# Kernel optimization log

Measured on AMD Instinct MI355X. Metric: run time of the kernel, lower is better.

The kernel has to match this reference:

```python
import jax, jax.numpy as jnp
import numpy as np

K = 20          # knn
EPS = 1e-5      # InstanceNorm2d eps
NEG_SLOPE = 0.2 # LeakyReLU slope


def setup_inputs() -> dict:
    key = jax.random.key(0)
    k1, k2 = jax.random.split(key)
    B, C, N = 4, 64, 4096
    out_dim, in_dim = 64, 2 * C
    batch = jax.random.normal(k1, (B, C, N), dtype=jnp.float32)
    # Conv2d(in_dim, out_dim, kernel_size=1, bias=False) weight, squeezed to [out,in]
    W = jax.random.normal(k2, (out_dim, in_dim), dtype=jnp.float32) * (1.0 / np.sqrt(in_dim))
    return {"batch": batch, "W": W}


def reference(batch, W):
    x = batch  # [B, C, N]
    # --- KNNGraph: pairwise squared distances + top-k nearest ---
    xx = jnp.sum(x * x, axis=1)                      # [B, N]
    inner = jnp.einsum('bcn,bcm->bnm', x, x)         # [B, N, N]
    neg_dist = -(xx[:, :, None] - 2.0 * inner + xx[:, None, :])  # [B, N, N]
    _, idx = jax.lax.top_k(neg_dist, K)              # [B, N, K] nearest neighbors
    # --- edge feature gather: concat(x_j - x_i, x_i) -> [B, 2C, N, K] ---
    nbr = jax.vmap(lambda xb, ib: xb[:, ib])(x, idx) # [B, C, N, K]
    center = x[:, :, :, None]                        # [B, C, N, 1]
    edge = jnp.concatenate([nbr - center, jnp.broadcast_to(center, nbr.shape)], axis=1)
    # --- 1x1 Conv2d (shared MLP, no bias) ---
    y = jnp.einsum('oc,bcnk->bonk', W, edge)         # [B, out, N, K]
    # --- InstanceNorm2d (no affine, biased var over spatial dims) ---
    mean = jnp.mean(y, axis=(2, 3), keepdims=True)
    var = jnp.var(y, axis=(2, 3), keepdims=True)
    y = (y - mean) * jax.lax.rsqrt(var + EPS)
    # --- LeakyReLU(0.2) ---
    y = jnp.where(y >= 0, y, NEG_SLOPE * y)
    # --- MaxPool over neighbor dim ---
    return jnp.max(y, axis=3)                        # [B, out, N]
```

## Files before the change

### kernel.cpp

```cpp
#include <hip/hip_runtime.h>
#include <hip/hip_bf16.h>
#include <cstdint>
#include <cstddef>

#define BB 4
#define NN 4096
#define NROW (BB*NN)
#define CAP3 512
#define ZSTAR 2.17f
#define SLACK 0.40

typedef float v2f   __attribute__((ext_vector_type(2)));
typedef float f32x16 __attribute__((ext_vector_type(16)));
typedef short s16x8 __attribute__((ext_vector_type(8)));
typedef _Float16 f16x8 __attribute__((ext_vector_type(8)));

__device__ __forceinline__ v2f pkfma(v2f a, v2f b, v2f c) {
  return __builtin_elementwise_fma(a, b, c);
}

__device__ __forceinline__ unsigned long long sort64(unsigned long long S, int lane) {
  #pragma unroll
  for (int kk = 2; kk <= 64; kk <<= 1) {
    #pragma unroll
    for (int j = kk >> 1; j > 0; j >>= 1) {
      unsigned long long o = __shfl_xor(S, j);
      bool up    = ((lane & kk) == 0);
      bool lower = ((lane & j) == 0);
      unsigned long long mn = (S < o) ? S : o;
      unsigned long long mx = (S < o) ? o : S;
      S = (lower == up) ? mn : mx;
    }
  }
  return S;
}
__device__ __forceinline__ unsigned long long merge_low64(
    unsigned long long L, unsigned long long S, int lane) {
  unsigned long long Sr = __shfl(S, 63 - lane);
  unsigned long long lo = (L < Sr) ? L : Sr;
  #pragma unroll
  for (int j = 32; j > 0; j >>= 1) {
    unsigned long long o = __shfl_xor(lo, j);
    unsigned long long mn = (lo < o) ? lo : o;
    unsigned long long mx = (lo < o) ? o : lo;
    lo = ((lane & j) == 0) ? mn : mx;
  }
  return lo;
}

__global__ __launch_bounds__(256) void k1_prep(
    const float* __restrict__ x, const float* __restrict__ W,
    float* __restrict__ xT, unsigned short* __restrict__ xh2,
    double* __restrict__ xxd, float* __restrict__ Trow,
    float* __restrict__ uT, float* __restrict__ vT)
{
  __shared__ float xc[64][65];
  __shared__ float xr[64][68];
  __shared__ float w1[64][65];
  __shared__ float wd[64][65];
  int t = threadIdx.x;
  int b  = blockIdx.x >> 6;
  int n0 = (blockIdx.x & 63) * 64;

  for (int i = t; i < 4096; i += 256) {
    int o = i >> 6, c = i & 63;
    float a = W[o*128 + c];
    w1[o][c] = a;
    wd[o][c] = W[o*128 + 64 + c] - a;
  }
  for (int i = t; i < 4096; i += 256) {
    int c = i >> 6, n = i & 63;
    xc[c][n] = x[((size_t)b*64 + c)*4096 + n0 + n];
  }
  __syncthreads();

  for (int i = t; i < 4096; i += 256) {
    int n = i >> 6, c = i & 63;
    float v = xc[c][n];
    xr[n][c] = v;
    size_t pt = (size_t)b*4096 + n0 + n;
    xT[pt*64 + c] = v;
    xh2[pt*80 + c] = __builtin_bit_cast(unsigned short, (_Float16)v);
  }
  if (t < 64) {
    int n = t;
    float s0=0,s1=0,s2=0,s3=0; double sd=0.0;
    for (int c = 0; c < 64; c += 4) {
      float a0=xc[c][n],a1=xc[c+1][n],a2=xc[c+2][n],a3=xc[c+3][n];
      s0=fmaf(a0,a0,s0); s1=fmaf(a1,a1,s1); s2=fmaf(a2,a2,s2); s3=fmaf(a3,a3,s3);
      sd += (double)a0*a0 + (double)a1*a1 + (double)a2*a2 + (double)a3*a3;
    }
    float xxv = (s0+s1)+(s2+s3);
    size_t ri = (size_t)b*4096 + n0 + n;
    xxd[ri] = sd;
    Trow[ri] = fmaf(-ZSTAR, sqrtf(fmaf(4.0f, xxv, 128.0f)), 64.0f);
    size_t xb2 = ri*80 + 64;
    xh2[xb2] = __builtin_bit_cast(unsigned short, (_Float16)xxv);
    #pragma unroll
    for (int q = 1; q < 16; ++q) xh2[xb2 + q] = 0;
  }
  v2f w1r[32], wdr[32];
  int o = t & 63;
  #pragma unroll
  for (int j = 0; j < 32; ++j) {
    w1r[j].x = w1[o][2*j]; w1r[j].y = w1[o][2*j+1];
    wdr[j].x = wd[o][2*j]; wdr[j].y = wd[o][2*j+1];
  }
  __syncthreads();

  for (int i = t; i < 4096; i += 256) {
    int n = i >> 6;
    v2f au; au.x=0.f; au.y=0.f;
    v2f av; av.x=0.f; av.y=0.f;
    #pragma unroll
    for (int cb = 0; cb < 16; ++cb) {
      float4 xv = *(const float4*)&xr[n][cb*4];
      v2f p0; p0.x = xv.x; p0.y = xv.y;
      v2f p1; p1.x = xv.z; p1.y = xv.w;
      au = pkfma(w1r[2*cb],   p0, au);
      au = pkfma(w1r[2*cb+1], p1, au);
      av = pkfma(wdr[2*cb],   p0, av);
      av = pkfma(wdr[2*cb+1], p1, av);
    }
    size_t idx = ((size_t)b*4096 + n0 + n)*64 + o;
    uT[idx] = au.x + au.y;
    vT[idx] = av.x + av.y;
  }
}

__global__ __launch_bounds__(256) void k2_screen(
    const unsigned short* __restrict__ xh2, const float* __restrict__ Trow,
    unsigned* __restrict__ bitmap)
{
  int t  = threadIdx.x;
  int nblk = blockIdx.x >> 3;
  int ms   = blockIdx.x & 7;
  int row0 = nblk * 128;
  int b = row0 >> 12;
  int wv = t >> 6, lane = t & 63;
  int lr = lane & 31, oct = lane >> 5;
  int n = row0 + wv*32 + lr;

  s16x8 bn[5];
  #pragma unroll
  for (int ks = 0; ks < 4; ++ks)
    bn[ks] = *(const s16x8*)(xh2 + (size_t)n*80 + ks*16 + oct*8);
  {
    s16x8 z;
    #pragma unroll
    for (int q = 0; q < 8; ++q) z[q] = 0;
    if (!oct) z[0] = (short)0xB800;
    bn[4] = z;
  }
  float cn = -0.5f * Trow[n];

  const unsigned short* xmB = xh2 + (size_t)b*4096*80;
  int mbase = ms * 512;

  for (int mt = 0; mt < 8; ++mt) {
    int m0 = mbase + mt*64;
    s16x8 am0[5], am1[5];
    #pragma unroll
    for (int ks = 0; ks < 4; ++ks) {
      am0[ks] = *(const s16x8*)(xmB + (size_t)(m0 + lr)*80      + ks*16 + oct*8);
      am1[ks] = *(const s16x8*)(xmB + (size_t)(m0 + 32 + lr)*80 + ks*16 + oct*8);
    }
    am0[4] = *(const s16x8*)(xmB + (size_t)(m0 + lr)*80      + 64 + oct*8);
    am1[4] = *(const s16x8*)(xmB + (size_t)(m0 + 32 + lr)*80 + 64 + oct*8);

    f32x16 a0, a1;
    #pragma unroll
    for (int i = 0; i < 16; ++i) { a0[i] = 0.f; a1[i] = 0.f; }
    #pragma unroll
    for (int ks = 0; ks < 5; ++ks) {
      f16x8 B = __builtin_bit_cast(f16x8, bn[ks]);
      a0 = __builtin_amdgcn_mfma_f32_32x32x16_f16(
             __builtin_bit_cast(f16x8, am0[ks]), B, a0, 0, 0, 0);
      a1 = __builtin_amdgcn_mfma_f32_32x32x16_f16(
             __builtin_bit_cast(f16x8, am1[ks]), B, a1, 0, 0, 0);
    }

    unsigned ua[4] = {0u,0u,0u,0u}, ub[4] = {0u,0u,0u,0u};
    #pragma unroll
    for (int i = 0; i < 16; ++i) {
      int p = (i & 3) + 8*(i >> 2) + 4*oct;
      unsigned bit = 1u << p;
      ua[i & 3] = (a0[i] > cn) ? (ua[i & 3] | bit) : ua[i & 3];
      ub[i & 3] = (a1[i] > cn) ? (ub[i & 3] | bit) : ub[i & 3];
    }
    unsigned u0 = (ua[0] | ua[1]) | (ua[2] | ua[3]);
    unsigned u1 = (ub[0] | ub[1]) | (ub[2] | ub[3]);
    unsigned w0 = u0 | (unsigned)__shfl_xor((int)u0, 32);
    unsigned w1 = u1 | (unsigned)__shfl_xor((int)u1, 32);
    bitmap[(size_t)n*128 + ms*16 + mt*2 + oct] = oct ? w1 : w0;
  }
}

__global__ __launch_bounds__(256) void k3_select(
    const float* __restrict__ xT, const double* __restrict__ xxd,
    const float* __restrict__ Trow, const unsigned* __restrict__ bitmap,
    const float* __restrict__ uT, const float* __restrict__ vT,
    float* __restrict__ stage, double* __restrict__ pS1, double* __restrict__ pS2,
    unsigned* __restrict__ slowcnt, unsigned* __restrict__ slowlist)
{
  __shared__ unsigned short candm[4][CAP3];
  int wv = threadIdx.x >> 6, lane = threadIdx.x & 63;
  int row = blockIdx.x * 4 + wv;
  int b = row >> 12;

  double s1t = 0.0, s2t = 0.0;
  double xxn = xxd[row];

  uint2 wds = *(const uint2*)&bitmap[(size_t)row*128 + lane*2];
  int myc = __popc(wds.x) + __popc(wds.y);
  int inc = myc;
  #pragma unroll
  for (int d = 1; d < 64; d <<= 1) {
    int v = __shfl_up(inc, d);
    if (lane >= d) inc += v;
  }
  int total = __shfl(inc, 63);
  int off = inc - myc;
  bool slow = (total < 20) || (total > CAP3);

  if (!slow) {
    unsigned w = wds.x; int mb = lane*64;
    while (w) { int j = __ffs(w) - 1; w &= w - 1;
                candm[wv][off++] = (unsigned short)(mb + j); }
    w = wds.y; mb = lane*64 + 32;
    while (w) { int j = __ffs(w) - 1; w &= w - 1;
                candm[wv][off++] = (unsigned short)(mb + j); }
  }
  __builtin_amdgcn_wave_barrier();

  if (!slow) {
    const float* pn = xT + (size_t)row*64;
    int nr = (total + 63) >> 6;
    unsigned long long L = ~0ull;
    for (int r = 0; r < nr; ++r) {
      int ci = r*64 + lane;
      unsigned long long S = ~0ull;
      if (ci < total) {
        int m = (int)candm[wv][ci];
        const float* pm = xT + ((size_t)b*4096 + m)*64;
        double acc0 = 0.0, acc1 = 0.0;
        #pragma unroll
        for (int c5 = 0; c5 < 64; c5 += 4) {
          float4 A = *(const float4*)(pn + c5);
          float4 B = *(const float4*)(pm + c5);
          acc0 = fma((double)A.x, (double)B.x, acc0);
          acc1 = fma((double)A.y, (double)B.y, acc1);
          acc0 = fma((double)A.z, (double)B.z, acc0);
          acc1 = fma((double)A.w, (double)B.w, acc1);
        }
        double d = xxn + xxd[(size_t)b*4096 + m] - 2.0*(acc0 + acc1);
        d = fmax(d, 0.0);
        S = (((unsigned long long)__double_as_longlong(d)) & ~0xFFFull)
          | (unsigned long long)m;
      }
      S = sort64(S, lane);
      L = (r == 0) ? S : merge_low64(L, S, lane);
    }
    unsigned long long k19 = __shfl(L, 19);
    double d20 = __longlong_as_double((long long)(k19 & ~0xFFFull));
    float Tr = Trow[row];
    if (!(d20 - xxn < (double)Tr - SLACK)) {
      slow = true;
    } else {
      int mlow = (int)(L & 0xFFFull);
      const float* ub = uT + (size_t)b*4096*64;
      float mx = -3.4e38f, s1 = 0.f, s2 = 0.f;
      #pragma unroll
      for (int k = 0; k < 20; ++k) {
        int m = __shfl(mlow, k);
        float g = ub[(size_t)m*64 + lane];
        mx = fmaxf(mx, g); s1 += g; s2 = fmaf(g, g, s2);
      }
      size_t ro = (size_t)row*64 + lane;
      float v = vT[ro];
      stage[ro] = mx + v;
      double dv = (double)v;
      s1t = (double)s1 + 20.0*dv;
      s2t = (double)s2 + 2.0*dv*(double)s1 + 20.0*dv*dv;
    }
  }
  if (slow && lane == 0) {
    unsigned i = atomicAdd(slowcnt, 1u); slowlist[i] = row;
  }
  pS1[(size_t)row*64 + lane] = s1t;
  pS2[(size_t)row*64 + lane] = s2t;
}

__global__ __launch_bounds__(256) void k3b_slow(
    const float* __restrict__ xT, const double* __restrict__ xxd,
    const unsigned* __restrict__ slowcnt, const unsigned* __restrict__ slowlist,
    const float* __restrict__ uT, const float* __restrict__ vT,
    float* __restrict__ stage, double* __restrict__ k3bS1, double* __restrict__ k3bS2)
{
  __shared__ unsigned long long wtop[4][64];
  __shared__ unsigned long long pend[4][64];
  __shared__ unsigned t20[20];
  unsigned nslow = *slowcnt;
  int t = threadIdx.x, wv = t >> 6, lane = t & 63;
  for (unsigned ii = blockIdx.x; ii < nslow; ii += gridDim.x) {
    int row = (int)slowlist[ii];
    int b = row >> 12, n = row & 4095;
    const float* pn = xT + ((size_t)b*4096 + n)*64;
    double xxn = xxd[(size_t)b*4096 + n];

    unsigned long long L;
    unsigned long long kth;
    int pc = 0;
    for (int r = 0; r < 16; ++r) {
      int m = wv*1024 + r*64 + lane;
      const float* pm = xT + ((size_t)b*4096 + m)*64;
      double acc0 = 0.0, acc1 = 0.0;
      #pragma unroll
      for (int c5 = 0; c5 < 64; c5 += 4) {
        float4 A = *(const float4*)(pn + c5);
        float4 B = *(const float4*)(pm + c5);
        acc0 = fma((double)A.x, (double)B.x, acc0);
        acc1 = fma((double)A.y, (double)B.y, acc1);
        acc0 = fma((double)A.z, (double)B.z, acc0);
        acc1 = fma((double)A.w, (double)B.w, acc1);
      }
      double d = xxn + xxd[(size_t)b*4096 + m] - 2.0*(acc0 + acc1);
      d = fmax(d, 0.0);
      unsigned long long S =
          (((unsigned long long)__double_as_longlong(d)) & ~0xFFFull)
        | (unsigned long long)m;
      if (r == 0) {
        L = sort64(S, lane);
        kth = __shfl(L, 63);
        continue;
      }
      bool take = (S < kth);
      unsigned long long mk = __ballot(take);
      int cnt = __popcll(mk);
      if (pc + cnt > 64) {
        __builtin_amdgcn_wave_barrier();
        unsigned long long P = (lane < pc) ? pend[wv][lane] : ~0ull;
        P = sort64(P, lane);
        L = merge_low64(L, P, lane);
        kth = __shfl(L, 63);
        pc = 0;
      }
      if (take) {
        int pos = pc + __popcll(mk & ((1ull << lane) - 1ull));
        pend[wv][pos] = S;
      }
      pc += cnt;
      __builtin_amdgcn_wave_barrier();
    }
    if (pc > 0) {
      __builtin_amdgcn_wave_barrier();
      unsigned long long P = (lane < pc) ? pend[wv][lane] : ~0ull;
      P = sort64(P, lane);
      L = merge_low64(L, P, lane);
    }
    wtop[wv][lane] = L;
    __syncthreads();
    if (wv == 0) {
      unsigned long long m01 = merge_low64(wtop[0][lane],
                                           wtop[1][lane], lane);
      unsigned long long m23 = merge_low64(wtop[2][lane],
                                           wtop[3][lane], lane);
      unsigned long long F = merge_low64(m01, m23, lane);
      if (lane < 20) t20[lane] = (unsigned)(F & 0xFFFull);
    }
    __syncthreads();
    if (t < 64) {
      const float* ub = uT + (size_t)b*4096*64;
      float mx = -3.4e38f, s1 = 0.f, s2 = 0.f;
      #pragma unroll
      for (int k = 0; k < 20; ++k) {
        unsigned m = t20[k];
        float g = ub[(size_t)m*64 + t];
        mx = fmaxf(mx, g); s1 += g; s2 = fmaf(g, g, s2);
      }
      size_t ro = ((size_t)b*4096 + n)*64 + t;
      float v = vT[ro];
      stage[ro] = mx + v;
      double dv = (double)v;
      __hip_atomic_fetch_add(&k3bS1[b*64 + t], (double)s1 + 20.0*dv,
                             __ATOMIC_RELAXED, __HIP_MEMORY_SCOPE_AGENT);
      __hip_atomic_fetch_add(&k3bS2[b*64 + t], (double)s2 + 2.0*dv*(double)s1 + 20.0*dv*dv,
                             __ATOMIC_RELAXED, __HIP_MEMORY_SCOPE_AGENT);
    }
    __syncthreads();
  }
}

__global__ __launch_bounds__(256) void k4a1_reduce(
    const double* __restrict__ pS1, const double* __restrict__ pS2,
    double* __restrict__ part1, double* __restrict__ part2)
{
  __shared__ double r1[4][64], r2[4][64];
  int blk = blockIdx.x;
  int t = threadIdx.x, wv = t >> 6, o = t & 63;
  size_t rbase = (size_t)blk*64 + wv*16;
  double s1 = 0.0, s2 = 0.0;
  for (int j = 0; j < 16; ++j) {
    s1 += pS1[(rbase + j)*64 + o];
    s2 += pS2[(rbase + j)*64 + o];
  }
  r1[wv][o] = s1; r2[wv][o] = s2;
  __syncthreads();
  if (wv == 0) {
    part1[(size_t)blk*64 + o] = r1[0][o]+r1[1][o]+r1[2][o]+r1[3][o];
    part2[(size_t)blk*64 + o] = r2[0][o]+r2[1][o]+r2[2][o]+r2[3][o];
  }
}

__global__ __launch_bounds__(256) void k4a2_params(
    const double* __restrict__ part1, const double* __restrict__ part2,
    const double* __restrict__ k3bS1, const double* __restrict__ k3bS2,
    float2* __restrict__ params)
{
  __shared__ double r1[4][64], r2[4][64];
  int b = blockIdx.x;
  int t = threadIdx.x, wv = t >> 6, o = t & 63;
  double s1 = 0.0, s2 = 0.0;
  for (int j = wv*16; j < wv*16 + 16; ++j) {
    s1 += part1[((size_t)b*64 + j)*64 + o];
    s2 += part2[((size_t)b*64 + j)*64 + o];
  }
  r1[wv][o] = s1; r2[wv][o] = s2;
  __syncthreads();
  if (wv == 0) {
    double S1 = k3bS1[b*64 + o] + r1[0][o]+r1[1][o]+r1[2][o]+r1[3][o];
    double S2 = k3bS2[b*64 + o] + r2[0][o]+r2[1][o]+r2[2][o]+r2[3][o];
    double inv = 1.0 / (4096.0 * 20.0);
    double mean = S1 * inv;
    double var  = S2 * inv - mean * mean;
    float2 pr; pr.x = (float)mean; pr.y = (float)rsqrt(var + 1e-5);
    params[b*64 + o] = pr;
  }
}

__global__ __launch_bounds__(256) void k4b_final(
    const float* __restrict__ stage, const float2* __restrict__ params,
    float* __restrict__ out)
{
  __shared__ float tile[64][65];
  int blk = blockIdx.x;
  int b = blk >> 6, n0 = (blk & 63) * 64;
  int t = threadIdx.x;
  int o = t & 63;
  float2 pr = params[b*64 + o];
  for (int i = t; i < 4096; i += 256) {
    int nn = i >> 6;
    float y = (stage[((size_t)b*4096 + n0 + nn)*64 + o] - pr.x) * pr.y;
    tile[nn][o] = (y >= 0.f) ? y : 0.2f * y;
  }
  __syncthreads();
  for (int i = t; i < 4096; i += 256) {
    int oo = i >> 6, nn = i & 63;
    out[((size_t)(b*64 + oo))*4096 + n0 + nn] = tile[nn][oo];
  }
}

extern "C" void kernel_launch(void* const* d_in, const int* in_sizes, int n_in,
                              void* d_out, int out_size, void* d_ws, size_t ws_size,
                              hipStream_t stream)
{
  (void)in_sizes; (void)n_in; (void)out_size; (void)ws_size;
  const float* x = (const float*)d_in[0];
  const float* W = (const float*)d_in[1];
  float* out = (float*)d_out;

  char* ws = (char*)d_ws;
  size_t off = 0;
  auto alloc = [&](size_t bytes) {
    char* p = ws + off;
    off = (off + bytes + 255) & ~(size_t)255;
    return p;
  };
  float*          uT       = (float*)         alloc((size_t)NROW*64*4);
  float*          vT       = (float*)         alloc((size_t)NROW*64*4);
  float*          xT       = (float*)         alloc((size_t)NROW*64*4);
  float*          stage    = (float*)         alloc((size_t)NROW*64*4);
  unsigned short* xh2      = (unsigned short*)alloc((size_t)NROW*80*2);
  double*         xxd      = (double*)        alloc((size_t)NROW*8);
  float*          Trow     = (float*)         alloc((size_t)NROW*4);
  double*         pS1      = (double*)        alloc((size_t)NROW*64*8);
  double*         pS2      = (double*)        alloc((size_t)NROW*64*8);
  double*         part1    = (double*)        alloc((size_t)256*64*8);
  double*         part2    = (double*)        alloc((size_t)256*64*8);
  unsigned*       bitmap   = (unsigned*)      alloc((size_t)NROW*128*4);
  float2*         params   = (float2*)        alloc(256*8);
  unsigned*       slowcnt  = (unsigned*)      alloc(256);
  double*         k3bS1    = (double*)        alloc(256*8);
  double*         k3bS2    = (double*)        alloc(256*8);
  unsigned*       slowlist = (unsigned*)      alloc((size_t)NROW*4);

  hipMemsetAsync(slowcnt, 0, 256 + 2048 + 2048, stream);

  k1_prep    <<<256,  256, 0, stream>>>(x, W, xT, xh2, xxd, Trow, uT, vT);
  k2_screen  <<<1024, 256, 0, stream>>>(xh2, Trow, bitmap);
  k3_select  <<<4096, 256, 0, stream>>>(xT, xxd, Trow, bitmap, uT, vT,
                                        stage, pS1, pS2, slowcnt, slowlist);
  k3b_slow   <<<512,  256, 0, stream>>>(xT, xxd, slowcnt, slowlist,
                                        uT, vT, stage, k3bS1, k3bS2);
  k4a1_reduce<<<256,  256, 0, stream>>>(pS1, pS2, part1, part2);
  k4a2_params<<<4,    256, 0, stream>>>(part1, part2, k3bS1, k3bS2, params);
  k4b_final  <<<256,  256, 0, stream>>>(stage, params, out);
}
```

Baseline: 150.3 us.

## Fold slow-path full scan into select kernel, drop separate slow kernel

The separate k3b_slow kernel, its slow-row list, atomics and memset are removed. Rows that fail the candidate screen now fall back inside k3_select to a per-wave full 4096-point scan using a threshold-filtered pending buffer. This saves one kernel launch, a memset and the atomic accumulation of statistics. The cost is that a slow row is now scanned by a single wave rather than a whole block, which can lengthen the tail if many rows fail. The candidate path also switches from sort-and-merge on every round to threshold filtering.

```diff
diff --git a/kernel.cpp b/kernel.cpp
--- a/kernel.cpp
+++ b/kernel.cpp
@@ -200,16 +200,16 @@
     const float* __restrict__ xT, const double* __restrict__ xxd,
     const float* __restrict__ Trow, const unsigned* __restrict__ bitmap,
     const float* __restrict__ uT, const float* __restrict__ vT,
-    float* __restrict__ stage, double* __restrict__ pS1, double* __restrict__ pS2,
-    unsigned* __restrict__ slowcnt, unsigned* __restrict__ slowlist)
+    float* __restrict__ stage, double* __restrict__ pS1, double* __restrict__ pS2)
 {
   __shared__ unsigned short candm[4][CAP3];
+  __shared__ unsigned long long pend[4][64];
   int wv = threadIdx.x >> 6, lane = threadIdx.x & 63;
   int row = blockIdx.x * 4 + wv;
   int b = row >> 12;
 
-  double s1t = 0.0, s2t = 0.0;
   double xxn = xxd[row];
+  const double* xxb = xxd + (size_t)b*4096;
 
   uint2 wds = *(const uint2*)&bitmap[(size_t)row*128 + lane*2];
   int myc = __popc(wds.x) + __popc(wds.y);
@@ -221,9 +221,9 @@
   }
   int total = __shfl(inc, 63);
   int off = inc - myc;
-  bool slow = (total < 20) || (total > CAP3);
-
-  if (!slow) {
+  bool fullscan = (total < 20) || (total > CAP3);
+
+  if (!fullscan) {
     unsigned w = wds.x; int mb = lane*64;
     while (w) { int j = __ffs(w) - 1; w &= w - 1;
                 candm[wv][off++] = (unsigned short)(mb + j); }
@@ -233,15 +233,20 @@
   }
   __builtin_amdgcn_wave_barrier();
 
-  if (!slow) {
-    const float* pn = xT + (size_t)row*64;
-    int nr = (total + 63) >> 6;
-    unsigned long long L = ~0ull;
+  const float* pn = xT + (size_t)row*64;
+  unsigned long long L = ~0ull;
+
+  for (int attempt = 0; attempt < 2; ++attempt) {
+    int ncand = fullscan ? 4096 : total;
+    int nr = (ncand + 63) >> 6;
+    unsigned long long kth = ~0ull;
+    int pc = 0;
+    L = ~0ull;
     for (int r = 0; r < nr; ++r) {
       int ci = r*64 + lane;
       unsigned long long S = ~0ull;
-      if (ci < total) {
-        int m = (int)candm[wv][ci];
+      if (ci < ncand) {
+        int m = fullscan ? ci : (int)candm[wv][ci];
         const float* pm = xT + ((size_t)b*4096 + m)*64;
         double acc0 = 0.0, acc1 = 0.0;
         #pragma unroll
@@ -253,82 +258,11 @@
           acc0 = fma((double)A.z, (double)B.z, acc0);
           acc1 = fma((double)A.w, (double)B.w, acc1);
         }
-        double d = xxn + xxd[(size_t)b*4096 + m] - 2.0*(acc0 + acc1);
+        double d = xxn + xxb[m] - 2.0*(acc0 + acc1);
         d = fmax(d, 0.0);
         S = (((unsigned long long)__double_as_longlong(d)) & ~0xFFFull)
           | (unsigned long long)m;
       }
-      S = sort64(S, lane);
-      L = (r == 0) ? S : merge_low64(L, S, lane);
-    }
-    unsigned long long k19 = __shfl(L, 19);
-    double d20 = __longlong_as_double((long long)(k19 & ~0xFFFull));
-    float Tr = Trow[row];
-    if (!(d20 - xxn < (double)Tr - SLACK)) {
-      slow = true;
-    } else {
-      int mlow = (int)(L & 0xFFFull);
-      const float* ub = uT + (size_t)b*4096*64;
-      float mx = -3.4e38f, s1 = 0.f, s2 = 0.f;
-      #pragma unroll
-      for (int k = 0; k < 20; ++k) {
-        int m = __shfl(mlow, k);
-        float g = ub[(size_t)m*64 + lane];
-        mx = fmaxf(mx, g); s1 += g; s2 = fmaf(g, g, s2);
-      }
-      size_t ro = (size_t)row*64 + lane;
-      float v = vT[ro];
-      stage[ro] = mx + v;
-      double dv = (double)v;
-      s1t = (double)s1 + 20.0*dv;
-      s2t = (double)s2 + 2.0*dv*(double)s1 + 20.0*dv*dv;
-    }
-  }
-  if (slow && lane == 0) {
-    unsigned i = atomicAdd(slowcnt, 1u); slowlist[i] = row;
-  }
-  pS1[(size_t)row*64 + lane] = s1t;
-  pS2[(size_t)row*64 + lane] = s2t;
-}
-
-__global__ __launch_bounds__(256) void k3b_slow(
-    const float* __restrict__ xT, const double* __restrict__ xxd,
-    const unsigned* __restrict__ slowcnt, const unsigned* __restrict__ slowlist,
-    const float* __restrict__ uT, const float* __restrict__ vT,
-    float* __restrict__ stage, double* __restrict__ k3bS1, double* __restrict__ k3bS2)
-{
-  __shared__ unsigned long long wtop[4][64];
-  __shared__ unsigned long long pend[4][64];
-  __shared__ unsigned t20[20];
-  unsigned nslow = *slowcnt;
-  int t = threadIdx.x, wv = t >> 6, lane = t & 63;
-  for (unsigned ii = blockIdx.x; ii < nslow; ii += gridDim.x) {
-    int row = (int)slowlist[ii];
-    int b = row >> 12, n = row & 4095;
-    const float* pn = xT + ((size_t)b*4096 + n)*64;
-    double xxn = xxd[(size_t)b*4096 + n];
-
-    unsigned long long L;
-    unsigned long long kth;
-    int pc = 0;
-    for (int r = 0; r < 16; ++r) {
-      int m = wv*1024 + r*64 + lane;
-      const float* pm = xT + ((size_t)b*4096 + m)*64;
-      double acc0 = 0.0, acc1 = 0.0;
-      #pragma unroll
-      for (int c5 = 0; c5 < 64; c5 += 4) {
-        float4 A = *(const float4*)(pn + c5);
-        float4 B = *(const float4*)(pm + c5);
-        acc0 = fma((double)A.x, (double)B.x, acc0);
-        acc1 = fma((double)A.y, (double)B.y, acc1);
-        acc0 = fma((double)A.z, (double)B.z, acc0);
-        acc1 = fma((double)A.w, (double)B.w, acc1);
-      }
-      double d = xxn + xxd[(size_t)b*4096 + m] - 2.0*(acc0 + acc1);
-      d = fmax(d, 0.0);
-      unsigned long long S =
-          (((unsigned long long)__double_as_longlong(d)) & ~0xFFFull)
-        | (unsigned long long)m;
       if (r == 0) {
         L = sort64(S, lane);
         kth = __shfl(L, 63);
@@ -358,37 +292,29 @@
       P = sort64(P, lane);
       L = merge_low64(L, P, lane);
     }
-    wtop[wv][lane] = L;
-    __syncthreads();
-    if (wv == 0) {
-      unsigned long long m01 = merge_low64(wtop[0][lane],
-                                           wtop[1][lane], lane);
-      unsigned long long m23 = merge_low64(wtop[2][lane],
-                                           wtop[3][lane], lane);
-      unsigned long long F = merge_low64(m01, m23, lane);
-      if (lane < 20) t20[lane] = (unsigned)(F & 0xFFFull);
-    }
-    __syncthreads();
-    if (t < 64) {
-      const float* ub = uT + (size_t)b*4096*64;
-      float mx = -3.4e38f, s1 = 0.f, s2 = 0.f;
-      #pragma unroll
-      for (int k = 0; k < 20; ++k) {
-        unsigned m = t20[k];
-        float g = ub[(size_t)m*64 + t];
-        mx = fmaxf(mx, g); s1 += g; s2 = fmaf(g, g, s2);
-      }
-      size_t ro = ((size_t)b*4096 + n)*64 + t;
-      float v = vT[ro];
-      stage[ro] = mx + v;
-      double dv = (double)v;
-      __hip_atomic_fetch_add(&k3bS1[b*64 + t], (double)s1 + 20.0*dv,
-                             __ATOMIC_RELAXED, __HIP_MEMORY_SCOPE_AGENT);
-      __hip_atomic_fetch_add(&k3bS2[b*64 + t], (double)s2 + 2.0*dv*(double)s1 + 20.0*dv*dv,
-                             __ATOMIC_RELAXED, __HIP_MEMORY_SCOPE_AGENT);
-    }
-    __syncthreads();
-  }
+    if (fullscan) break;
+    unsigned long long k19 = __shfl(L, 19);
+    double d20 = __longlong_as_double((long long)(k19 & ~0xFFFull));
+    float Tr = Trow[row];
+    if (d20 - xxn < (double)Tr - SLACK) break;
+    fullscan = true;
+  }
+
+  int mlow = (int)(L & 0xFFFull);
+  const float* ub = uT + (size_t)b*4096*64;
+  float mx = -3.4e38f, s1 = 0.f, s2 = 0.f;
+  #pragma unroll
+  for (int k = 0; k < 20; ++k) {
+    int m = __shfl(mlow, k);
+    float g = ub[(size_t)m*64 + lane];
+    mx = fmaxf(mx, g); s1 += g; s2 = fmaf(g, g, s2);
+  }
+  size_t ro = (size_t)row*64 + lane;
+  float v = vT[ro];
+  stage[ro] = mx + v;
+  double dv = (double)v;
+  pS1[ro] = (double)s1 + 20.0*dv;
+  pS2[ro] = (double)s2 + 2.0*dv*(double)s1 + 20.0*dv*dv;
 }
 
 __global__ __launch_bounds__(256) void k4a1_reduce(
@@ -414,7 +340,6 @@
 
 __global__ __launch_bounds__(256) void k4a2_params(
     const double* __restrict__ part1, const double* __restrict__ part2,
-    const double* __restrict__ k3bS1, const double* __restrict__ k3bS2,
     float2* __restrict__ params)
 {
   __shared__ double r1[4][64], r2[4][64];
@@ -428,8 +353,8 @@
   r1[wv][o] = s1; r2[wv][o] = s2;
   __syncthreads();
   if (wv == 0) {
-    double S1 = k3bS1[b*64 + o] + r1[0][o]+r1[1][o]+r1[2][o]+r1[3][o];
-    double S2 = k3bS2[b*64 + o] + r2[0][o]+r2[1][o]+r2[2][o]+r2[3][o];
+    double S1 = r1[0][o]+r1[1][o]+r1[2][o]+r1[3][o];
+    double S2 = r2[0][o]+r2[1][o]+r2[2][o]+r2[3][o];
     double inv = 1.0 / (4096.0 * 20.0);
     double mean = S1 * inv;
     double var  = S2 * inv - mean * mean;
@@ -489,20 +414,12 @@
   double*         part2    = (double*)        alloc((size_t)256*64*8);
   unsigned*       bitmap   = (unsigned*)      alloc((size_t)NROW*128*4);
   float2*         params   = (float2*)        alloc(256*8);
-  unsigned*       slowcnt  = (unsigned*)      alloc(256);
-  double*         k3bS1    = (double*)        alloc(256*8);
-  double*         k3bS2    = (double*)        alloc(256*8);
-  unsigned*       slowlist = (unsigned*)      alloc((size_t)NROW*4);
-
-  hipMemsetAsync(slowcnt, 0, 256 + 2048 + 2048, stream);
 
   k1_prep    <<<256,  256, 0, stream>>>(x, W, xT, xh2, xxd, Trow, uT, vT);
   k2_screen  <<<1024, 256, 0, stream>>>(xh2, Trow, bitmap);
   k3_select  <<<4096, 256, 0, stream>>>(xT, xxd, Trow, bitmap, uT, vT,
-                                        stage, pS1, pS2, slowcnt, slowlist);
-  k3b_slow   <<<512,  256, 0, stream>>>(xT, xxd, slowcnt, slowlist,
-                                        uT, vT, stage, k3bS1, k3bS2);
+                                        stage, pS1, pS2);
   k4a1_reduce<<<256,  256, 0, stream>>>(pS1, pS2, part1, part2);
-  k4a2_params<<<4,    256, 0, stream>>>(part1, part2, k3bS1, k3bS2, params);
+  k4a2_params<<<4,    256, 0, stream>>>(part1, part2, params);
   k4b_final  <<<256,  256, 0, stream>>>(stage, params, out);
 }
```

Result: slower. 223.5 us (+48.7%).
